# Optimization experiments

Hardware: AMD Instinct MI355X
Metric: run time of the kernel (lower is better)

## Reference

```python
import jax, jax.numpy as jnp
import numpy as np

EPS = 1e-7


def _project_to_ball(x, max_norm=0.9):
    # keep points strictly inside the unit Poincare ball
    n = jnp.linalg.norm(x, axis=-1, keepdims=True)
    return x * (max_norm / (1.0 + n))


def _poincare_pairwise_dist(x, y, c=1.0):
    # x: (B, d), y: (L, d) -> (B, L) hyperbolic distances
    x2 = jnp.sum(x * x, axis=-1, keepdims=True)            # (B, 1)
    y2 = jnp.sum(y * y, axis=-1, keepdims=True).T          # (1, L)
    xy = x @ y.T                                           # (B, L) GEMM
    sq = jnp.maximum(x2 + y2 - 2.0 * xy, 0.0)              # ||x - y||^2
    denom = jnp.maximum((1.0 - c * x2) * (1.0 - c * y2), EPS)
    arg = jnp.maximum(1.0 + 2.0 * c * sq / denom, 1.0 + EPS)
    return jnp.arccosh(arg) / jnp.sqrt(c)


def setup_inputs() -> dict:
    key = jax.random.key(0)
    k1, k2 = jax.random.split(key)
    z_hyp = _project_to_ball(jax.random.normal(k1, (4096, 256), dtype=jnp.float32))
    leaf_emb = _project_to_ball(jax.random.normal(k2, (50000, 256), dtype=jnp.float32))
    leaf_node_ids = jnp.arange(50000, dtype=jnp.int32)
    threshold = jnp.ones((), dtype=jnp.float32)
    return {"z_hyp": z_hyp, "leaf_emb": leaf_emb,
            "leaf_node_ids": leaf_node_ids, "threshold": threshold}


def reference(z_hyp, leaf_emb, leaf_node_ids, threshold):
    c = 1.0
    dists = _poincare_pairwise_dist(z_hyp, leaf_emb, c)      # (B, L)
    scores = jnp.min(dists, axis=-1)                          # (B,) OOD score
    is_ood = scores > threshold                               # (B,) bool
    k = min(5, leaf_emb.shape[0])
    # topk smallest distances -> negate and take top_k
    _, topk = jax.lax.top_k(-dists, k)                        # (B, 5)
    topk_ids = leaf_node_ids[topk]                            # (B, 5)
    return scores, is_ood, topk_ids
```

## Files before the change

### kernel.cpp

```cpp
#include <hip/hip_runtime.h>
#include <hip/hip_bf16.h>
#include <float.h>
#include <stdint.h>

#define BATCH 4096
#define NLEAF 50000
#define DIM   256
#define BN    128
#define NTILES 391
#define NGRP  (NTILES * 8)
#define MAXC  128
#define NCHUNK 8
#define GPC   ((NGRP + NCHUNK - 1) / NCHUNK)

typedef _Float16 h8  __attribute__((ext_vector_type(8)));
typedef float    f16v __attribute__((ext_vector_type(16)));

__device__ __forceinline__ void insert5v(float key, float (&k)[5]) {
    if (key < k[4]) {
        if (key < k[3]) { k[4]=k[3];
            if (key < k[2]) { k[3]=k[2];
                if (key < k[1]) { k[2]=k[1];
                    if (key < k[0]) { k[1]=k[0]; k[0]=key; } else k[1]=key;
                } else k[2]=key;
            } else k[3]=key;
        } else k[4]=key;
    }
}

__device__ __forceinline__ bool lexless(float k, int i, float K, int I) {
    return (k < K) || (k == K && i < I);
}
__device__ __forceinline__ void insert5lex(float key, int id, float (&k)[5], int (&ix)[5]) {
    if (lexless(key, id, k[4], ix[4])) {
        if (lexless(key, id, k[3], ix[3])) { k[4]=k[3]; ix[4]=ix[3];
            if (lexless(key, id, k[2], ix[2])) { k[3]=k[2]; ix[3]=ix[2];
                if (lexless(key, id, k[1], ix[1])) { k[2]=k[1]; ix[2]=ix[1];
                    if (lexless(key, id, k[0], ix[0])) { k[1]=k[0]; ix[1]=ix[0]; k[0]=key; ix[0]=id; }
                    else { k[1]=key; ix[1]=id; }
                } else { k[2]=key; ix[2]=id; }
            } else { k[3]=key; ix[3]=id; }
        } else { k[4]=key; ix[4]=id; }
    }
}

__device__ __forceinline__ void gload_lds16(const void* g, void* l) {
    __builtin_amdgcn_global_load_lds(
        (const __attribute__((address_space(1))) uint32_t*)g,
        (__attribute__((address_space(3))) uint32_t*)l, 16, 0, 0);
}

__global__ void norms_cvt_k(const float* __restrict__ z, const float* __restrict__ leaf,
                            float* __restrict__ x2, float* __restrict__ afac,
                            float* __restrict__ y2, float* __restrict__ bfac,
                            unsigned short* __restrict__ zf, unsigned short* __restrict__ lf) {
    int wv = (blockIdx.x * 256 + threadIdx.x) >> 6;
    int l = threadIdx.x & 63;
    if (wv >= BATCH + NLEAF) return;
    bool isz = wv < BATCH;
    const float* row = isz ? z + (size_t)wv * DIM : leaf + (size_t)(wv - BATCH) * DIM;
    float4 v = reinterpret_cast<const float4*>(row)[l];
    _Float16 h0 = (_Float16)v.x, h1 = (_Float16)v.y, h2 = (_Float16)v.z, h3 = (_Float16)v.w;
    ushort4 u;
    u.x = __builtin_bit_cast(unsigned short, h0);
    u.y = __builtin_bit_cast(unsigned short, h1);
    u.z = __builtin_bit_cast(unsigned short, h2);
    u.w = __builtin_bit_cast(unsigned short, h3);
    unsigned short* dst = isz ? zf + (size_t)wv * DIM : lf + (size_t)(wv - BATCH) * DIM;
    reinterpret_cast<ushort4*>(dst)[l] = u;
    float s = v.x*v.x + v.y*v.y + v.z*v.z + v.w*v.w;
#pragma unroll
    for (int off = 32; off > 0; off >>= 1) s += __shfl_down(s, off, 64);
    if (l == 0) {
        if (isz) { x2[wv] = s; afac[wv] = 2.0f / (1.0f - s); }
        else { int j = wv - BATCH; y2[j] = s; bfac[j] = 1.0f / (1.0f - s); }
    }
}

__global__ __launch_bounds__(256, 2) void gemm_min_k(
        const unsigned short* __restrict__ zf, const unsigned short* __restrict__ lf,
        const float* __restrict__ x2, const float* __restrict__ y2,
        const float* __restrict__ bfac, float* __restrict__ mins) {
    extern __shared__ char sm[];
    float2* ybt = (float2*)(sm + 65536);
    float*  xt  = (float*)(sm + 66560);

    const int t = threadIdx.x;
    const int w = t >> 6, l = t & 63;
    const int wr = w >> 1, wc = w & 1;
    const int l31 = l & 31, lg2 = l >> 5;

    const int bid = blockIdx.x;
    const int xcd = bid & 7, q = bid >> 3;
    const int ntile = xcd * 49 + (q >> 5);
    if (ntile >= NTILES) return;
    const int m0 = (q & 31) * 128;
    const int l0 = ntile * BN;

    if (t < 128) {
        xt[t] = x2[m0 + t];
        int gl = l0 + t;
        bool v = gl < NLEAF;
        float bb = v ? bfac[gl] : 0.0f;
        float yy = v ? y2[gl] : 0.0f;
        ybt[t] = make_float2(bb, v ? yy * bb : 1e30f);
    }

    int srcA[4], srcB[4];
#pragma unroll
    for (int j = 0; j < 4; ++j) {
        int slot = j * 256 + t;
        int row = slot >> 3, sl = slot & 7;
        int swz = sl ^ (row & 7);
        srcA[j] = (m0 + row) * 512 + swz * 16;
        int gl = l0 + row; if (gl > NLEAF - 1) gl = NLEAF - 1;
        srcB[j] = gl * 512 + swz * 16;
    }

    f16v acc[2][2];
#pragma unroll
    for (int i = 0; i < 2; ++i)
#pragma unroll
        for (int j = 0; j < 2; ++j)
#pragma unroll
            for (int r = 0; r < 16; ++r) acc[i][j][r] = 0.0f;

    auto stage = [&](int ks, int bsel) {
        char* dst = sm + bsel * 32768;
        const int kb = ks * 128;
#pragma unroll
        for (int j = 0; j < 4; ++j) {
            gload_lds16((const char*)zf + srcA[j] + kb, dst + (j * 256 + w * 64) * 16);
            gload_lds16((const char*)lf + srcB[j] + kb, dst + 16384 + (j * 256 + w * 64) * 16);
        }
    };

    auto compute = [&](int bsel) {
        const char* Ab = sm + bsel * 32768;
        const char* Bb = Ab + 16384;
#pragma unroll
        for (int kk = 0; kk < 4; ++kk) {
            const int cz = kk * 32 + lg2 * 16;
            h8 za[2], lb[2];
#pragma unroll
            for (int f = 0; f < 2; ++f) {
                int ra = wr * 64 + f * 32 + l31;
                za[f] = *(const h8*)(Ab + ra * 128 + (cz ^ ((ra & 7) << 4)));
                int rb = wc * 64 + f * 32 + l31;
                lb[f] = *(const h8*)(Bb + rb * 128 + (cz ^ ((rb & 7) << 4)));
            }
#pragma unroll
            for (int fi = 0; fi < 2; ++fi)
#pragma unroll
                for (int fj = 0; fj < 2; ++fj)
                    acc[fi][fj] = __builtin_amdgcn_mfma_f32_32x32x16_f16(lb[fj], za[fi], acc[fi][fj], 0, 0, 0);
        }
    };

    stage(0, 0);
    __syncthreads();
#pragma unroll
    for (int ks = 0; ks < 4; ++ks) {
        if (ks < 3) stage(ks + 1, (ks + 1) & 1);
        compute(ks & 1);
        __syncthreads();
    }

    float xv[2] = { xt[wr * 64 + l31], xt[wr * 64 + 32 + l31] };
#pragma unroll
    for (int fi = 0; fi < 2; ++fi)
#pragma unroll
        for (int fj = 0; fj < 2; ++fj)
#pragma unroll
            for (int hi = 0; hi < 2; ++hi) {
                float kx[8];
#pragma unroll
                for (int r8 = 0; r8 < 8; ++r8) {
                    int reg = hi * 8 + r8;
                    int L = wc * 64 + fj * 32 + (r8 & 3) + 8 * (r8 >> 2) + 4 * lg2 + 16 * hi;
                    float2 p = ybt[L];
                    float a = acc[fi][fj][reg];
                    kx[r8] = fmaf(p.x, fmaf(-2.0f, a, xv[fi]), p.y);
                }
                float gm = fminf(fminf(fminf(kx[0], kx[1]), fminf(kx[2], kx[3])),
                                 fminf(fminf(kx[4], kx[5]), fminf(kx[6], kx[7])));
                gm = fminf(gm, __shfl_xor(gm, 32, 64));
                if (lg2 == 0) {
                    int g = ntile * 8 + wc * 4 + fj * 2 + hi;
                    mins[(size_t)g * BATCH + m0 + wr * 64 + fi * 32 + l31] = gm;
                }
            }
}

__global__ __launch_bounds__(256) void select1_k(const float* __restrict__ mins,
                                                 float* __restrict__ part5) {
    __shared__ float sm5[4][64][5];
    const int w = threadIdx.x >> 6, l = threadIdx.x & 63;
    const int row = blockIdx.x * 64 + l;
    const int jb = w * ((GPC + 3) / 4);
    const int je = min(GPC, jb + (GPC + 3) / 4);
    float t5[5] = {FLT_MAX, FLT_MAX, FLT_MAX, FLT_MAX, FLT_MAX};
    int j = jb;
    for (; j + 4 <= je; j += 4) {
        int g = blockIdx.y * GPC + j;
        float a0 = (g     < NGRP) ? mins[(size_t)g * BATCH + row] : FLT_MAX;
        float a1 = (g + 1 < NGRP) ? mins[(size_t)(g + 1) * BATCH + row] : FLT_MAX;
        float a2 = (g + 2 < NGRP) ? mins[(size_t)(g + 2) * BATCH + row] : FLT_MAX;
        float a3 = (g + 3 < NGRP) ? mins[(size_t)(g + 3) * BATCH + row] : FLT_MAX;
        insert5v(a0, t5); insert5v(a1, t5); insert5v(a2, t5); insert5v(a3, t5);
    }
    for (; j < je; ++j) {
        int g = blockIdx.y * GPC + j;
        float a = (g < NGRP) ? mins[(size_t)g * BATCH + row] : FLT_MAX;
        insert5v(a, t5);
    }
#pragma unroll
    for (int q = 0; q < 5; ++q) sm5[w][l][q] = t5[q];
    __syncthreads();
    if (w == 0) {
#pragma unroll
        for (int ww = 1; ww < 4; ++ww)
#pragma unroll
            for (int q = 0; q < 5; ++q) insert5v(sm5[ww][l][q], t5);
#pragma unroll
        for (int q = 0; q < 5; ++q)
            part5[((size_t)row * NCHUNK + blockIdx.y) * 5 + q] = t5[q];
    }
}

__global__ void select_merge_k(const float* __restrict__ part5,
                               float* __restrict__ rowthr, int* __restrict__ cnt) {
    int row = blockIdx.x * 256 + threadIdx.x;
    if (row >= BATCH) return;
    float t5[5] = {FLT_MAX, FLT_MAX, FLT_MAX, FLT_MAX, FLT_MAX};
    const float* p = part5 + (size_t)row * NCHUNK * 5;
    for (int s = 0; s < NCHUNK * 5; ++s) insert5v(p[s], t5);
    rowthr[row] = t5[4] + 2e-3f * fabsf(t5[4]) + 2.5e-2f;
    cnt[row] = 0;
}

__global__ __launch_bounds__(256) void select_scan_k(const float* __restrict__ mins,
                                                     const float* __restrict__ rowthr,
                                                     int* __restrict__ cnt,
                                                     int* __restrict__ cand) {
    const int w = threadIdx.x >> 6, l = threadIdx.x & 63;
    const int row = blockIdx.x * 64 + l;
    const float thr = rowthr[row];
    const int jb = w * ((GPC + 3) / 4);
    const int je = min(GPC, jb + (GPC + 3) / 4);
    for (int j = jb; j < je; ++j) {
        int g = blockIdx.y * GPC + j;
        if (g >= NGRP) break;
        float m = mins[(size_t)g * BATCH + row];
        if (m <= thr) {
            int c = atomicAdd(&cnt[row], 1);
            if (c < MAXC) cand[row * MAXC + c] = g;
        }
    }
}

__global__ __launch_bounds__(256) void recheck_k(
        const float* __restrict__ z, const float* __restrict__ leaf,
        const float* __restrict__ x2, const float* __restrict__ y2,
        const float* __restrict__ bfac, const float* __restrict__ afac,
        const int* __restrict__ cnt, const int* __restrict__ cand,
        const int* __restrict__ ids, const float* __restrict__ thr,
        float* __restrict__ out) {
    __shared__ float mk[20];
    __shared__ int   mi[20];
    const int row = blockIdx.x;
    const int t = threadIdx.x, w = t >> 6, l = t & 63;
    float4 zr = *(const float4*)(z + (size_t)row * DIM + l * 4);
    const float x2r = x2[row];
    int nc = cnt[row]; if (nc > MAXC) nc = MAXC;
    float k5[5]; int i5[5];
#pragma unroll
    for (int q = 0; q < 5; ++q) { k5[q] = FLT_MAX; i5[q] = 0x7FFFFFFF; }
    for (int ci = w; ci < nc; ci += 4) {
        int g = cand[row * MAXC + ci];
#pragma unroll 1
        for (int jj = 0; jj < 16; ++jj) {
            int id = g * 16 + jj;
            if (id >= NLEAF) break;
            float4 lfv = *(const float4*)(leaf + (size_t)id * DIM + l * 4);
            float d = zr.x * lfv.x;
            d = fmaf(zr.y, lfv.y, d); d = fmaf(zr.z, lfv.z, d); d = fmaf(zr.w, lfv.w, d);
#pragma unroll
            for (int s = 1; s < 64; s <<= 1) d += __shfl_xor(d, s, 64);
            float sq = fmaxf(x2r + y2[id] - 2.0f * d, 0.0f);
            float key = sq * bfac[id];
            insert5lex(key, id, k5, i5);
        }
    }
    if (l == 0) {
#pragma unroll
        for (int q = 0; q < 5; ++q) { mk[w * 5 + q] = k5[q]; mi[w * 5 + q] = i5[q]; }
    }
    __syncthreads();
    if (t == 0) {
        float fk[5]; int fi[5];
#pragma unroll
        for (int q = 0; q < 5; ++q) { fk[q] = FLT_MAX; fi[q] = 0x7FFFFFFF; }
        for (int s = 0; s < 20; ++s) insert5lex(mk[s], mi[s], fk, fi);
        float u = fk[0] * afac[row];
        u = fmaxf(u, 1e-7f);
        float dd = log1pf(u + sqrtf(u * (u + 2.0f)));
        out[row] = dd;
        out[BATCH + row] = (dd > thr[0]) ? 1.0f : 0.0f;
#pragma unroll
        for (int q = 0; q < 5; ++q)
            out[2 * BATCH + (size_t)row * 5 + q] = (float)ids[fi[q]];
    }
}

extern "C" void kernel_launch(void* const* d_in, const int* in_sizes, int n_in,
                              void* d_out, int out_size, void* d_ws, size_t ws_size,
                              hipStream_t stream) {
    const float* z    = (const float*)d_in[0];
    const float* leaf = (const float*)d_in[1];
    const int*   ids  = (const int*)d_in[2];
    const float* thr  = (const float*)d_in[3];
    float* out = (float*)d_out;

    char* ws = (char*)d_ws;
    float* x2   = (float*)(ws + 0);
    float* afac = (float*)(ws + 16384);
    float* y2   = (float*)(ws + 32768);
    float* bfac = (float*)(ws + 232768);
    unsigned short* zf = (unsigned short*)(ws + 432768);
    unsigned short* lf = (unsigned short*)(ws + 2529920);
    float* mins = (float*)(ws + 28129920);
    int* cnt  = (int*)(ws + 79379072);
    int* cand = (int*)(ws + 79395456);
    float* part5  = (float*)(ws + 81492608);
    float* rowthr = (float*)(ws + 82147968);

    norms_cvt_k<<<(BATCH + NLEAF + 3) / 4, 256, 0, stream>>>(z, leaf, x2, afac, y2, bfac, zf, lf);
    gemm_min_k<<<8 * 49 * 32, 256, 67072, stream>>>(zf, lf, x2, y2, bfac, mins);
    select1_k<<<dim3(BATCH / 64, NCHUNK), 256, 0, stream>>>(mins, part5);
    select_merge_k<<<(BATCH + 255) / 256, 256, 0, stream>>>(part5, rowthr, cnt);
    select_scan_k<<<dim3(BATCH / 64, NCHUNK), 256, 0, stream>>>(mins, rowthr, cnt, cand);
    recheck_k<<<BATCH, 256, 0, stream>>>(z, leaf, x2, y2, bfac, afac, cnt, cand, ids, thr, out);
}
```

Measured before the change: 393.6 us.

## Store per-group minima in fp16 and widen recheck to 512 threads

```diff
diff --git a/kernel.cpp b/kernel.cpp
--- a/kernel.cpp
+++ b/kernel.cpp
@@ -15,6 +15,10 @@
 
 typedef _Float16 h8  __attribute__((ext_vector_type(8)));
 typedef float    f16v __attribute__((ext_vector_type(16)));
+
+__device__ __forceinline__ float h2f(unsigned short u) {
+    return (float)__builtin_bit_cast(_Float16, u);
+}
 
 __device__ __forceinline__ void insert5v(float key, float (&k)[5]) {
     if (key < k[4]) {
@@ -80,7 +84,7 @@
 __global__ __launch_bounds__(256, 2) void gemm_min_k(
         const unsigned short* __restrict__ zf, const unsigned short* __restrict__ lf,
         const float* __restrict__ x2, const float* __restrict__ y2,
-        const float* __restrict__ bfac, float* __restrict__ mins) {
+        const float* __restrict__ bfac, unsigned short* __restrict__ mins) {
     extern __shared__ char sm[];
     float2* ybt = (float2*)(sm + 65536);
     float*  xt  = (float*)(sm + 66560);
@@ -187,12 +191,14 @@
                 gm = fminf(gm, __shfl_xor(gm, 32, 64));
                 if (lg2 == 0) {
                     int g = ntile * 8 + wc * 4 + fj * 2 + hi;
-                    mins[(size_t)g * BATCH + m0 + wr * 64 + fi * 32 + l31] = gm;
+                    _Float16 hgm = (_Float16)fminf(gm, 60000.0f);
+                    mins[(size_t)g * BATCH + m0 + wr * 64 + fi * 32 + l31] =
+                        __builtin_bit_cast(unsigned short, hgm);
                 }
             }
 }
 
-__global__ __launch_bounds__(256) void select1_k(const float* __restrict__ mins,
+__global__ __launch_bounds__(256) void select1_k(const unsigned short* __restrict__ mins,
                                                  float* __restrict__ part5) {
     __shared__ float sm5[4][64][5];
     const int w = threadIdx.x >> 6, l = threadIdx.x & 63;
@@ -203,15 +209,18 @@
     int j = jb;
     for (; j + 4 <= je; j += 4) {
         int g = blockIdx.y * GPC + j;
-        float a0 = (g     < NGRP) ? mins[(size_t)g * BATCH + row] : FLT_MAX;
-        float a1 = (g + 1 < NGRP) ? mins[(size_t)(g + 1) * BATCH + row] : FLT_MAX;
-        float a2 = (g + 2 < NGRP) ? mins[(size_t)(g + 2) * BATCH + row] : FLT_MAX;
-        float a3 = (g + 3 < NGRP) ? mins[(size_t)(g + 3) * BATCH + row] : FLT_MAX;
-        insert5v(a0, t5); insert5v(a1, t5); insert5v(a2, t5); insert5v(a3, t5);
+        float a0 = (g     < NGRP) ? h2f(mins[(size_t)g * BATCH + row]) : FLT_MAX;
+        float a1 = (g + 1 < NGRP) ? h2f(mins[(size_t)(g + 1) * BATCH + row]) : FLT_MAX;
+        float a2 = (g + 2 < NGRP) ? h2f(mins[(size_t)(g + 2) * BATCH + row]) : FLT_MAX;
+        float a3 = (g + 3 < NGRP) ? h2f(mins[(size_t)(g + 3) * BATCH + row]) : FLT_MAX;
+        float m4 = fminf(fminf(a0, a1), fminf(a2, a3));
+        if (m4 < t5[4]) {
+            insert5v(a0, t5); insert5v(a1, t5); insert5v(a2, t5); insert5v(a3, t5);
+        }
     }
     for (; j < je; ++j) {
         int g = blockIdx.y * GPC + j;
-        float a = (g < NGRP) ? mins[(size_t)g * BATCH + row] : FLT_MAX;
+        float a = (g < NGRP) ? h2f(mins[(size_t)g * BATCH + row]) : FLT_MAX;
         insert5v(a, t5);
     }
 #pragma unroll
@@ -235,11 +244,11 @@
     float t5[5] = {FLT_MAX, FLT_MAX, FLT_MAX, FLT_MAX, FLT_MAX};
     const float* p = part5 + (size_t)row * NCHUNK * 5;
     for (int s = 0; s < NCHUNK * 5; ++s) insert5v(p[s], t5);
-    rowthr[row] = t5[4] + 2e-3f * fabsf(t5[4]) + 2.5e-2f;
+    rowthr[row] = t5[4] + 2e-3f * fabsf(t5[4]) + 1.8e-2f;
     cnt[row] = 0;
 }
 
-__global__ __launch_bounds__(256) void select_scan_k(const float* __restrict__ mins,
+__global__ __launch_bounds__(256) void select_scan_k(const unsigned short* __restrict__ mins,
                                                      const float* __restrict__ rowthr,
                                                      int* __restrict__ cnt,
                                                      int* __restrict__ cand) {
@@ -251,7 +260,7 @@
     for (int j = jb; j < je; ++j) {
         int g = blockIdx.y * GPC + j;
         if (g >= NGRP) break;
-        float m = mins[(size_t)g * BATCH + row];
+        float m = h2f(mins[(size_t)g * BATCH + row]);
         if (m <= thr) {
             int c = atomicAdd(&cnt[row], 1);
             if (c < MAXC) cand[row * MAXC + c] = g;
@@ -259,15 +268,15 @@
     }
 }
 
-__global__ __launch_bounds__(256) void recheck_k(
+__global__ __launch_bounds__(512) void recheck_k(
         const float* __restrict__ z, const float* __restrict__ leaf,
         const float* __restrict__ x2, const float* __restrict__ y2,
         const float* __restrict__ bfac, const float* __restrict__ afac,
         const int* __restrict__ cnt, const int* __restrict__ cand,
         const int* __restrict__ ids, const float* __restrict__ thr,
         float* __restrict__ out) {
-    __shared__ float mk[20];
-    __shared__ int   mi[20];
+    __shared__ float mk[40];
+    __shared__ int   mi[40];
     const int row = blockIdx.x;
     const int t = threadIdx.x, w = t >> 6, l = t & 63;
     float4 zr = *(const float4*)(z + (size_t)row * DIM + l * 4);
@@ -276,20 +285,20 @@
     float k5[5]; int i5[5];
 #pragma unroll
     for (int q = 0; q < 5; ++q) { k5[q] = FLT_MAX; i5[q] = 0x7FFFFFFF; }
-    for (int ci = w; ci < nc; ci += 4) {
+    for (int ci = w; ci < nc; ci += 8) {
         int g = cand[row * MAXC + ci];
-#pragma unroll 1
+#pragma unroll 4
         for (int jj = 0; jj < 16; ++jj) {
             int id = g * 16 + jj;
-            if (id >= NLEAF) break;
-            float4 lfv = *(const float4*)(leaf + (size_t)id * DIM + l * 4);
+            int idc = (id < NLEAF) ? id : (NLEAF - 1);
+            float4 lfv = *(const float4*)(leaf + (size_t)idc * DIM + l * 4);
             float d = zr.x * lfv.x;
             d = fmaf(zr.y, lfv.y, d); d = fmaf(zr.z, lfv.z, d); d = fmaf(zr.w, lfv.w, d);
 #pragma unroll
             for (int s = 1; s < 64; s <<= 1) d += __shfl_xor(d, s, 64);
-            float sq = fmaxf(x2r + y2[id] - 2.0f * d, 0.0f);
-            float key = sq * bfac[id];
-            insert5lex(key, id, k5, i5);
+            float sq = fmaxf(x2r + y2[idc] - 2.0f * d, 0.0f);
+            float key = (id < NLEAF) ? sq * bfac[idc] : FLT_MAX;
+            insert5lex(key, (id < NLEAF) ? id : 0x7FFFFFFF, k5, i5);
         }
     }
     if (l == 0) {
@@ -301,7 +310,7 @@
         float fk[5]; int fi[5];
 #pragma unroll
         for (int q = 0; q < 5; ++q) { fk[q] = FLT_MAX; fi[q] = 0x7FFFFFFF; }
-        for (int s = 0; s < 20; ++s) insert5lex(mk[s], mi[s], fk, fi);
+        for (int s = 0; s < 40; ++s) insert5lex(mk[s], mi[s], fk, fi);
         float u = fk[0] * afac[row];
         u = fmaxf(u, 1e-7f);
         float dd = log1pf(u + sqrtf(u * (u + 2.0f)));
@@ -329,7 +338,7 @@
     float* bfac = (float*)(ws + 232768);
     unsigned short* zf = (unsigned short*)(ws + 432768);
     unsigned short* lf = (unsigned short*)(ws + 2529920);
-    float* mins = (float*)(ws + 28129920);
+    unsigned short* mins = (unsigned short*)(ws + 28129920);
     int* cnt  = (int*)(ws + 79379072);
     int* cand = (int*)(ws + 79395456);
     float* part5  = (float*)(ws + 81492608);
@@ -340,5 +349,5 @@
     select1_k<<<dim3(BATCH / 64, NCHUNK), 256, 0, stream>>>(mins, part5);
     select_merge_k<<<(BATCH + 255) / 256, 256, 0, stream>>>(part5, rowthr, cnt);
     select_scan_k<<<dim3(BATCH / 64, NCHUNK), 256, 0, stream>>>(mins, rowthr, cnt, cand);
-    recheck_k<<<BATCH, 256, 0, stream>>>(z, leaf, x2, y2, bfac, afac, cnt, cand, ids, thr, out);
-}
+    recheck_k<<<BATCH, 512, 0, stream>>>(z, leaf, x2, y2, bfac, afac, cnt, cand, ids, thr, out);
+}
```

New measurement: 434.9 us. 1.1x slower.
